# Performance work log

Hardware: AMD Instinct MI355X
Metric: run time of the kernel (lower is better)

The kernel has to match this reference:

```python
import jax, jax.numpy as jnp
import numpy as np

B, T, D, H, C = 256, 512, 300, 128, 6

def setup_inputs() -> dict:
    key = jax.random.key(0)
    ks = jax.random.split(key, 8)
    s = 1.0 / np.sqrt(H)  # PyTorch LSTM/Linear uniform init scale
    x = jax.random.normal(ks[0], (B, T, D), dtype=jnp.float32)
    lengths = jax.random.randint(ks[1], (B,), 1, T + 1)
    W_ih = jax.random.uniform(ks[2], (4 * H, D), minval=-s, maxval=s, dtype=jnp.float32)
    W_hh = jax.random.uniform(ks[3], (4 * H, H), minval=-s, maxval=s, dtype=jnp.float32)
    b_ih = jax.random.uniform(ks[4], (4 * H,), minval=-s, maxval=s, dtype=jnp.float32)
    b_hh = jax.random.uniform(ks[5], (4 * H,), minval=-s, maxval=s, dtype=jnp.float32)
    fc_w = jax.random.uniform(ks[6], (C, H), minval=-s, maxval=s, dtype=jnp.float32)
    fc_b = jax.random.uniform(ks[7], (C,), minval=-s, maxval=s, dtype=jnp.float32)
    return {"x": x, "W_ih": W_ih, "W_hh": W_hh, "b_ih": b_ih, "b_hh": b_hh,
            "fc_w": fc_w, "fc_b": fc_b, "lengths": lengths}

def _lstm_last_hidden(x, W_ih, W_hh, b_ih, b_hh, lengths):
    # Equivalent to pack_padded_sequence + nn.LSTM: the returned hidden[-1]
    # is the state at t = length-1 for each sequence. We run a masked scan:
    # state updates are frozen once t >= length.
    Bv, Tv, _ = x.shape
    Hv = W_hh.shape[1]
    xs = jnp.swapaxes(x, 0, 1)                              # [T, B, D]
    gx = jnp.einsum('tbd,gd->tbg', xs, W_ih) + b_ih + b_hh  # [T, B, 4H]
    mask = (jnp.arange(Tv)[:, None] < lengths[None, :])     # [T, B]

    def step(carry, inp):
        h, c = carry
        g, m = inp
        gates = g + h @ W_hh.T                              # [B, 4H]
        i, f, gg, o = jnp.split(gates, 4, axis=-1)          # PyTorch gate order i,f,g,o
        i = jax.nn.sigmoid(i)
        f = jax.nn.sigmoid(f)
        gg = jnp.tanh(gg)
        o = jax.nn.sigmoid(o)
        c_new = f * c + i * gg
        h_new = o * jnp.tanh(c_new)
        m = m[:, None]
        h = jnp.where(m, h_new, h)
        c = jnp.where(m, c_new, c)
        return (h, c), None

    h0 = jnp.zeros((Bv, Hv), dtype=x.dtype)
    c0 = jnp.zeros((Bv, Hv), dtype=x.dtype)
    (h, c), _ = jax.lax.scan(step, (h0, c0), (gx, mask))
    return h

def reference(x, W_ih, W_hh, b_ih, b_hh, fc_w, fc_b, lengths):
    h = _lstm_last_hidden(x, W_ih, W_hh, b_ih, b_hh, lengths)  # [B, H]
    return h @ fc_w.T + fc_b                                   # [B, 6]
```

## Files before the change

### kernel.cpp

```cpp
#include <hip/hip_runtime.h>
#include <hip/hip_bf16.h>
#include <stdint.h>
#include <type_traits>

#define NB 256
#define NT 512
#define ND 300
#define NH 128
#define NG 512
#define NC 6

typedef __attribute__((ext_vector_type(8))) short short8;
typedef __attribute__((ext_vector_type(4))) float f32x4;

#if __has_builtin(__builtin_amdgcn_fdot2_f32_bf16)
#define HAS_DOT2 1
typedef __attribute__((ext_vector_type(2))) __bf16 bf16x2_t;
static __device__ __forceinline__ float dot2bf(unsigned int wp, unsigned int hp, float acc) {
  return __builtin_amdgcn_fdot2_f32_bf16(__builtin_bit_cast(bf16x2_t, wp),
                                         __builtin_bit_cast(bf16x2_t, hp), acc, false);
}
#else
static __device__ __forceinline__ float dot2bf(unsigned int wp, unsigned int hp, float acc) {
  float wl = __builtin_bit_cast(float, wp << 16);
  float wh = __builtin_bit_cast(float, wp & 0xffff0000u);
  float hl = __builtin_bit_cast(float, hp << 16);
  float hh = __builtin_bit_cast(float, hp & 0xffff0000u);
  return fmaf(wh, hh, fmaf(wl, hl, acc));
}
#endif

static __device__ __forceinline__ float bf2f(unsigned int u) {
  return __builtin_bit_cast(float, (u & 0xffffu) << 16);
}
static __device__ __forceinline__ unsigned short f2bf(float f) {
  return __builtin_bit_cast(unsigned short, __float2bfloat16(f));
}
static __device__ __forceinline__ unsigned int packbf(float a, float b) {
  return (unsigned int)f2bf(a) | ((unsigned int)f2bf(b) << 16);
}
static __device__ __forceinline__ float ld1(const unsigned short* p) { return bf2f(*p); }
static __device__ __forceinline__ float ld1(const float* p) { return *p; }
static __device__ __forceinline__ void st1(unsigned short* p, float v) { *p = f2bf(v); }
static __device__ __forceinline__ void st1(float* p, float v) { *p = v; }

static __device__ __forceinline__ float tanh_fast(float x) {
  return 1.f - 2.f * __builtin_amdgcn_rcpf(__expf(2.f * x) + 1.f);
}

static __device__ __forceinline__ uint2 load4bf(const unsigned short* row, int k, int lim) {
  uint2 v;
  if (k + 3 < lim) {
    v = *(const uint2*)(row + k);
  } else {
    unsigned int e0 = (k + 0 < lim) ? row[k + 0] : 0;
    unsigned int e1 = (k + 1 < lim) ? row[k + 1] : 0;
    unsigned int e2 = (k + 2 < lim) ? row[k + 2] : 0;
    unsigned int e3 = (k + 3 < lim) ? row[k + 3] : 0;
    v.x = e0 | (e1 << 16);
    v.y = e2 | (e3 << 16);
  }
  return v;
}
static __device__ __forceinline__ uint2 load4bf(const float* row, int k, int lim) {
  float f0 = 0.f, f1 = 0.f, f2 = 0.f, f3 = 0.f;
  if (k + 3 < lim) {
    float4 f = *(const float4*)(row + k);
    f0 = f.x; f1 = f.y; f2 = f.z; f3 = f.w;
  } else {
    if (k + 0 < lim) f0 = row[k + 0];
    if (k + 1 < lim) f1 = row[k + 1];
    if (k + 2 < lim) f2 = row[k + 2];
    if (k + 3 < lim) f3 = row[k + 3];
  }
  uint2 v;
  v.x = packbf(f0, f1);
  v.y = packbf(f2, f3);
  return v;
}

__global__ void detect_dtype(const unsigned short* __restrict__ X, int* __restrict__ flag) {
  __shared__ int cnt;
  if (threadIdx.x == 0) cnt = 0;
  __syncthreads();
  int c = 0;
  for (int i = threadIdx.x; i < 512; i += 64) {
    unsigned int u = X[i];
    unsigned int e = (u >> 7) & 0xffu;
    if (u == 0u || (e >= 97u && e <= 157u)) c++;
  }
  atomicAdd(&cnt, c);
  __syncthreads();
  if (threadIdx.x == 0) *flag = (cnt >= 448) ? 0 : 1;
}

template <typename XT, typename GXT>
__global__ __launch_bounds__(256) void gx_gemm(const int* __restrict__ flag, int want,
                                               const XT* __restrict__ X,
                                               const XT* __restrict__ Wih,
                                               const int* __restrict__ lengths,
                                               GXT* __restrict__ gx,
                                               int b_base, int t_base, int Tc) {
  if (*flag != want) return;
  const int mb = blockIdx.x;
  const int m0 = mb << 7;
  const int bc = m0 / Tc;
  const int trel0 = m0 % Tc;
  const int b = b_base + bc;
  const int t0 = t_base + trel0;
  const int len = lengths[b];
  if (t0 >= len) return;

  __shared__ unsigned short As[128][40];
  __shared__ unsigned short Bs[64][40];

  const int tid = threadIdx.x;
  const int lane = tid & 63;
  const int wave = tid >> 6;
  const int wm = wave & 1;
  const int wn = wave >> 1;
  const int lq = lane >> 4;
  const int lr = lane & 15;

  const int rA = tid >> 1, cA = (tid & 1) * 16;
  const int rB = tid >> 2, cB = (tid & 3) * 8;
  const XT* xrow = X + ((size_t)b * NT + t0 + rA) * ND;

  for (int nt = 0; nt < 8; ++nt) {
    const int n0 = nt << 6;
    const XT* wrow = Wih + (size_t)(n0 + rB) * ND;

    f32x4 acc[4][2];
#pragma unroll
    for (int i = 0; i < 4; ++i)
#pragma unroll
      for (int j = 0; j < 2; ++j) {
        f32x4 z = {0.f, 0.f, 0.f, 0.f};
        acc[i][j] = z;
      }

    for (int kc = 0; kc < 320; kc += 32) {
      __syncthreads();
#pragma unroll
      for (int g4 = 0; g4 < 4; ++g4)
        *(uint2*)&As[rA][cA + g4 * 4] = load4bf(xrow, kc + cA + g4 * 4, ND);
#pragma unroll
      for (int g4 = 0; g4 < 2; ++g4)
        *(uint2*)&Bs[rB][cB + g4 * 4] = load4bf(wrow, kc + cB + g4 * 4, ND);
      __syncthreads();

      short8 af[4], bq[2];
#pragma unroll
      for (int tm = 0; tm < 4; ++tm)
        af[tm] = *(const short8*)&As[wm * 64 + tm * 16 + lr][lq * 8];
#pragma unroll
      for (int tn = 0; tn < 2; ++tn)
        bq[tn] = *(const short8*)&Bs[wn * 32 + tn * 16 + lr][lq * 8];
#pragma unroll
      for (int tm = 0; tm < 4; ++tm)
#pragma unroll
        for (int tn = 0; tn < 2; ++tn)
          acc[tm][tn] =
              __builtin_amdgcn_mfma_f32_16x16x32_bf16(af[tm], bq[tn], acc[tm][tn], 0, 0, 0);
    }

#pragma unroll
    for (int tm = 0; tm < 4; ++tm)
#pragma unroll
      for (int tn = 0; tn < 2; ++tn)
#pragma unroll
        for (int rg = 0; rg < 4; ++rg) {
          const int tileRow = wm * 64 + tm * 16 + lq * 4 + rg;
          if (t0 + tileRow < len) {
            const int col = n0 + wn * 32 + tn * 16 + lr;
            st1(gx + (size_t)(m0 + tileRow) * NG + col, acc[tm][tn][rg]);
          }
        }
  }
}

template <typename XT, typename GXT>
__global__ __launch_bounds__(512, 2) void lstm_rec(const int* __restrict__ flag, int want,
                                                   const GXT* __restrict__ gx,
                                                   const XT* __restrict__ Whh,
                                                   const XT* __restrict__ bih,
                                                   const XT* __restrict__ bhh,
                                                   const XT* __restrict__ fcw,
                                                   const XT* __restrict__ fcb,
                                                   const int* __restrict__ lengths,
                                                   XT* __restrict__ out,
                                                   float* __restrict__ hstate,
                                                   float* __restrict__ cstate,
                                                   int b_base, int t_base, int Tc) {
  if (*flag != want) return;
  const int bc = blockIdx.x;
  const int b = b_base + bc;
  int len = lengths[b];
  if (len > NT) len = NT;
  if (len < 0) len = 0;
  const bool first = (t_base == 0);
  const bool last = (t_base + Tc >= NT);
  const int tend = (len < t_base + Tc) ? len : (t_base + Tc);
  if (!last && tend <= t_base) return;

  const int tid = threadIdx.x;
  const int w8 = tid >> 6;
  const int l = tid & 63;
  const int g = l >> 4;
  const int unit = w8 * 16 + (l & 15);
  const int row = g * NH + unit;

  __shared__ __align__(16) unsigned short hpk[2][NH];
  __shared__ __align__(16) float hf[NH];

  unsigned int w2[64];
  if constexpr (std::is_same_v<XT, unsigned short>) {
    const uint4* wp = (const uint4*)Whh + (size_t)row * 16;
#pragma unroll
    for (int i = 0; i < 16; ++i) {
      uint4 v = wp[i];
      w2[4 * i + 0] = v.x;
      w2[4 * i + 1] = v.y;
      w2[4 * i + 2] = v.z;
      w2[4 * i + 3] = v.w;
    }
  } else {
    const float4* wp = (const float4*)(Whh + (size_t)row * NH);
#pragma unroll
    for (int i = 0; i < 32; ++i) {
      float4 v = wp[i];
      w2[2 * i + 0] = packbf(v.x, v.y);
      w2[2 * i + 1] = packbf(v.z, v.w);
    }
  }

  const float bias = ld1(bih + row) + ld1(bhh + row);
  const bool isg = (g == 2);
  const float Au = isg ? 1.f : 0.f;
  const float Bu = isg ? -2.f : 1.f;
  const float Mu = isg ? 2.f : -1.f;

  float hcur = 0.f, ccur = 0.f;
  if (!first) {
    hcur = hstate[(size_t)bc * NH + unit];
    ccur = cstate[(size_t)bc * NH + unit];
  }
  if (g == 0) hpk[0][unit] = f2bf(hcur);
  __syncthreads();

  const GXT* gxc = gx + (size_t)bc * Tc * NG + row;
  const int nsteps = tend - t_base;
  float g_cur = (0 < nsteps) ? ld1(gxc) : 0.f;
  float g_n1 = (1 < nsteps) ? ld1(gxc + NG) : 0.f;

  for (int s = 0; s < nsteps; ++s) {
    float g_n2 = (s + 2 < nsteps) ? ld1(gxc + (size_t)(s + 2) * NG) : 0.f;

    const uint4* hb = (const uint4*)hpk[s & 1];
    float a0 = 0.f, a1 = 0.f, a2 = 0.f, a3 = 0.f;
#pragma unroll
    for (int i = 0; i < 16; ++i) {
      uint4 hv = hb[i];
      a0 = dot2bf(w2[4 * i + 0], hv.x, a0);
      a1 = dot2bf(w2[4 * i + 1], hv.y, a1);
      a2 = dot2bf(w2[4 * i + 2], hv.z, a2);
      a3 = dot2bf(w2[4 * i + 3], hv.w, a3);
    }
    const float gate = g_cur + bias + ((a0 + a1) + (a2 + a3));
    const float v = fmaf(Bu, __builtin_amdgcn_rcpf(__expf(Mu * gate) + 1.f), Au);

    const float x1 = __shfl_xor(v, 16, 64);
    const float x2 = __shfl_xor(v, 32, 64);
    const float x3 = __shfl_xor(x1, 32, 64);
    ccur = fmaf(x1, ccur, v * x2);
    hcur = x3 * tanh_fast(ccur);
    if (g == 0) hpk[(s + 1) & 1][unit] = f2bf(hcur);
    __syncthreads();

    g_cur = g_n1;
    g_n1 = g_n2;
  }

  if (!last) {
    if (g == 0) {
      hstate[(size_t)bc * NH + unit] = hcur;
      cstate[(size_t)bc * NH + unit] = ccur;
    }
  } else {
    if (g == 0) hf[unit] = hcur;
    __syncthreads();
    if (tid < NC) {
      float acc = ld1(fcb + tid);
      const XT* wv = fcw + (size_t)tid * NH;
#pragma unroll
      for (int k = 0; k < NH; ++k) acc = fmaf(ld1(wv + k), hf[k], acc);
      st1(out + (size_t)b * NC + tid, acc);
    }
  }
}

template <typename XT, typename GXT>
static void run_variant(int want, const int* flag, void* const* d_in, XT* out,
                        GXT* gx, float* hstate, float* cstate, int NBc, int Tc,
                        hipStream_t stream) {
  const XT* X = (const XT*)d_in[0];
  const XT* Wih = (const XT*)d_in[1];
  const XT* Whh = (const XT*)d_in[2];
  const XT* bih = (const XT*)d_in[3];
  const XT* bhh = (const XT*)d_in[4];
  const XT* fcw = (const XT*)d_in[5];
  const XT* fcb = (const XT*)d_in[6];
  const int* lengths = (const int*)d_in[7];
  for (int bb = 0; bb < NB; bb += NBc) {
    for (int tb = 0; tb < NT; tb += Tc) {
      gx_gemm<XT, GXT><<<dim3((NBc * Tc) / 128), dim3(256), 0, stream>>>(
          flag, want, X, Wih, lengths, gx, bb, tb, Tc);
      lstm_rec<XT, GXT><<<dim3(NBc), dim3(512), 0, stream>>>(
          flag, want, gx, Whh, bih, bhh, fcw, fcb, lengths, out, hstate, cstate, bb, tb, Tc);
    }
  }
}

extern "C" void kernel_launch(void* const* d_in, const int* in_sizes, int n_in,
                              void* d_out, int out_size, void* d_ws, size_t ws_size,
                              hipStream_t stream) {
  int* flag = (int*)d_ws;
  detect_dtype<<<dim3(1), dim3(64), 0, stream>>>((const unsigned short*)d_in[0], flag);

  const size_t full_f32 = (size_t)NB * NT * NG * sizeof(float);
  const size_t full_bf16 = (size_t)NB * NT * NG * 2;
  const size_t base = 512;

  int NBc, Tc;
  char* gx_raw;
  float* hstate = (float*)((char*)d_ws + base);
  bool gx_is_f32;

  if (ws_size >= base + full_f32) {
    NBc = NB; Tc = NT; gx_is_f32 = true;
    gx_raw = (char*)d_ws + base;
  } else if (ws_size >= base + full_bf16) {
    NBc = NB; Tc = NT; gx_is_f32 = false;
    gx_raw = (char*)d_ws + base;
  } else {
    Tc = 128; gx_is_f32 = false;
    NBc = 1;
    for (int cand : {64, 16, 4}) {
      size_t need = base + (size_t)cand * NH * 2 * sizeof(float) + (size_t)cand * Tc * NG * 2;
      if (ws_size >= need) { NBc = cand; break; }
    }
    gx_raw = (char*)d_ws + base + (size_t)NBc * NH * 2 * sizeof(float);
  }
  float* cstate = hstate + (size_t)NBc * NH;

  if (gx_is_f32) {
    run_variant<unsigned short, float>(0, flag, d_in, (unsigned short*)d_out,
                                       (float*)gx_raw, hstate, cstate, NBc, Tc, stream);
    run_variant<float, float>(1, flag, d_in, (float*)d_out, (float*)gx_raw, hstate,
                              cstate, NBc, Tc, stream);
  } else {
    run_variant<unsigned short, unsigned short>(0, flag, d_in, (unsigned short*)d_out,
                                                (unsigned short*)gx_raw, hstate, cstate,
                                                NBc, Tc, stream);
    run_variant<float, unsigned short>(1, flag, d_in, (float*)d_out,
                                       (unsigned short*)gx_raw, hstate, cstate, NBc, Tc,
                                       stream);
  }
}
```

Baseline: 668.7 us.

## Use MFMA for recurrent h·W_hh matvec and register-prefetch input GEMM tiles

The recurrent step now computes the h·W_hh product with 16x16x32 bf16 MFMA instructions. The W_hh fragments stay in registers, and the broadcast h is the B operand, so 15 of its 16 columns do redundant work. Each lane now holds all four gates for four hidden units, which removes the cross-lane shuffles; gate inputs are loaded as vectors. The input-projection GEMM also prefetches the next K-chunk into registers before the MFMA work, overlapping global loads with compute. This trades dot2 ALU work for wasted MFMA columns and more activation math per lane.

```diff
diff --git a/kernel.cpp b/kernel.cpp
--- a/kernel.cpp
+++ b/kernel.cpp
@@ -13,23 +13,6 @@
 typedef __attribute__((ext_vector_type(8))) short short8;
 typedef __attribute__((ext_vector_type(4))) float f32x4;
 
-#if __has_builtin(__builtin_amdgcn_fdot2_f32_bf16)
-#define HAS_DOT2 1
-typedef __attribute__((ext_vector_type(2))) __bf16 bf16x2_t;
-static __device__ __forceinline__ float dot2bf(unsigned int wp, unsigned int hp, float acc) {
-  return __builtin_amdgcn_fdot2_f32_bf16(__builtin_bit_cast(bf16x2_t, wp),
-                                         __builtin_bit_cast(bf16x2_t, hp), acc, false);
-}
-#else
-static __device__ __forceinline__ float dot2bf(unsigned int wp, unsigned int hp, float acc) {
-  float wl = __builtin_bit_cast(float, wp << 16);
-  float wh = __builtin_bit_cast(float, wp & 0xffff0000u);
-  float hl = __builtin_bit_cast(float, hp << 16);
-  float hh = __builtin_bit_cast(float, hp & 0xffff0000u);
-  return fmaf(wh, hh, fmaf(wl, hl, acc));
-}
-#endif
-
 static __device__ __forceinline__ float bf2f(unsigned int u) {
   return __builtin_bit_cast(float, (u & 0xffffu) << 16);
 }
@@ -44,39 +27,57 @@
 static __device__ __forceinline__ void st1(unsigned short* p, float v) { *p = f2bf(v); }
 static __device__ __forceinline__ void st1(float* p, float v) { *p = v; }
 
+static __device__ __forceinline__ float sigmoid_fast(float x) {
+  return __builtin_amdgcn_rcpf(1.f + __expf(-x));
+}
 static __device__ __forceinline__ float tanh_fast(float x) {
   return 1.f - 2.f * __builtin_amdgcn_rcpf(__expf(2.f * x) + 1.f);
 }
 
+static __device__ __forceinline__ uint2 load4bf_fast(const unsigned short* row, int k) {
+  return *(const uint2*)(row + k);
+}
+static __device__ __forceinline__ uint2 load4bf_fast(const float* row, int k) {
+  float4 f = *(const float4*)(row + k);
+  uint2 v;
+  v.x = packbf(f.x, f.y);
+  v.y = packbf(f.z, f.w);
+  return v;
+}
 static __device__ __forceinline__ uint2 load4bf(const unsigned short* row, int k, int lim) {
+  if (k + 3 < lim) return load4bf_fast(row, k);
+  unsigned int e0 = (k + 0 < lim) ? row[k + 0] : 0;
+  unsigned int e1 = (k + 1 < lim) ? row[k + 1] : 0;
+  unsigned int e2 = (k + 2 < lim) ? row[k + 2] : 0;
+  unsigned int e3 = (k + 3 < lim) ? row[k + 3] : 0;
   uint2 v;
-  if (k + 3 < lim) {
-    v = *(const uint2*)(row + k);
-  } else {
-    unsigned int e0 = (k + 0 < lim) ? row[k + 0] : 0;
-    unsigned int e1 = (k + 1 < lim) ? row[k + 1] : 0;
-    unsigned int e2 = (k + 2 < lim) ? row[k + 2] : 0;
-    unsigned int e3 = (k + 3 < lim) ? row[k + 3] : 0;
-    v.x = e0 | (e1 << 16);
-    v.y = e2 | (e3 << 16);
-  }
+  v.x = e0 | (e1 << 16);
+  v.y = e2 | (e3 << 16);
   return v;
 }
 static __device__ __forceinline__ uint2 load4bf(const float* row, int k, int lim) {
-  float f0 = 0.f, f1 = 0.f, f2 = 0.f, f3 = 0.f;
-  if (k + 3 < lim) {
-    float4 f = *(const float4*)(row + k);
-    f0 = f.x; f1 = f.y; f2 = f.z; f3 = f.w;
-  } else {
-    if (k + 0 < lim) f0 = row[k + 0];
-    if (k + 1 < lim) f1 = row[k + 1];
-    if (k + 2 < lim) f2 = row[k + 2];
-    if (k + 3 < lim) f3 = row[k + 3];
-  }
+  if (k + 3 < lim) return load4bf_fast(row, k);
+  float f0 = (k + 0 < lim) ? row[k + 0] : 0.f;
+  float f1 = (k + 1 < lim) ? row[k + 1] : 0.f;
+  float f2 = (k + 2 < lim) ? row[k + 2] : 0.f;
+  float f3 = (k + 3 < lim) ? row[k + 3] : 0.f;
   uint2 v;
   v.x = packbf(f0, f1);
   v.y = packbf(f2, f3);
   return v;
+}
+
+static __device__ __forceinline__ f32x4 ldgx4(const unsigned short* p) {
+  uint2 v = *(const uint2*)p;
+  f32x4 r;
+  r[0] = bf2f(v.x);
+  r[1] = bf2f(v.x >> 16);
+  r[2] = bf2f(v.y);
+  r[3] = bf2f(v.y >> 16);
+  return r;
+}
+static __device__ __forceinline__ f32x4 ldgx4(const float* p) {
+  return *(const f32x4*)p;
 }
 
 __global__ void detect_dtype(const unsigned short* __restrict__ X, int* __restrict__ flag) {
@@ -139,15 +140,35 @@
         acc[i][j] = z;
       }
 
-    for (int kc = 0; kc < 320; kc += 32) {
+    uint2 av[4], bv[2];
+#pragma unroll
+    for (int g4 = 0; g4 < 4; ++g4) av[g4] = load4bf_fast(xrow, cA + g4 * 4);
+#pragma unroll
+    for (int g4 = 0; g4 < 2; ++g4) bv[g4] = load4bf_fast(wrow, cB + g4 * 4);
+
+#pragma unroll
+    for (int kc9 = 0; kc9 < 10; ++kc9) {
       __syncthreads();
 #pragma unroll
-      for (int g4 = 0; g4 < 4; ++g4)
-        *(uint2*)&As[rA][cA + g4 * 4] = load4bf(xrow, kc + cA + g4 * 4, ND);
-#pragma unroll
-      for (int g4 = 0; g4 < 2; ++g4)
-        *(uint2*)&Bs[rB][cB + g4 * 4] = load4bf(wrow, kc + cB + g4 * 4, ND);
+      for (int g4 = 0; g4 < 4; ++g4) *(uint2*)&As[rA][cA + g4 * 4] = av[g4];
+#pragma unroll
+      for (int g4 = 0; g4 < 2; ++g4) *(uint2*)&Bs[rB][cB + g4 * 4] = bv[g4];
       __syncthreads();
+
+      if (kc9 < 9) {
+        const int kn = (kc9 + 1) * 32;
+        if (kc9 < 8) {
+#pragma unroll
+          for (int g4 = 0; g4 < 4; ++g4) av[g4] = load4bf_fast(xrow, kn + cA + g4 * 4);
+#pragma unroll
+          for (int g4 = 0; g4 < 2; ++g4) bv[g4] = load4bf_fast(wrow, kn + cB + g4 * 4);
+        } else {
+#pragma unroll
+          for (int g4 = 0; g4 < 4; ++g4) av[g4] = load4bf(xrow, kn + cA + g4 * 4, ND);
+#pragma unroll
+          for (int g4 = 0; g4 < 2; ++g4) bv[g4] = load4bf(wrow, kn + cB + g4 * 4, ND);
+        }
+      }
 
       short8 af[4], bq[2];
 #pragma unroll
@@ -202,92 +223,137 @@
   const bool last = (t_base + Tc >= NT);
   const int tend = (len < t_base + Tc) ? len : (t_base + Tc);
   if (!last && tend <= t_base) return;
+  int nsteps = tend - t_base;
+  if (nsteps < 0) nsteps = 0;
 
   const int tid = threadIdx.x;
   const int w8 = tid >> 6;
   const int l = tid & 63;
-  const int g = l >> 4;
-  const int unit = w8 * 16 + (l & 15);
-  const int row = g * NH + unit;
+  const int q = l >> 4;
+  const int m = l & 15;
+  const int u0 = w8 * 16 + q * 4;
 
   __shared__ __align__(16) unsigned short hpk[2][NH];
   __shared__ __align__(16) float hf[NH];
 
-  unsigned int w2[64];
-  if constexpr (std::is_same_v<XT, unsigned short>) {
-    const uint4* wp = (const uint4*)Whh + (size_t)row * 16;
-#pragma unroll
-    for (int i = 0; i < 16; ++i) {
-      uint4 v = wp[i];
-      w2[4 * i + 0] = v.x;
-      w2[4 * i + 1] = v.y;
-      w2[4 * i + 2] = v.z;
-      w2[4 * i + 3] = v.w;
-    }
+  short8 afr[4][4];
+#pragma unroll
+  for (int g = 0; g < 4; ++g) {
+    const int row = g * NH + w8 * 16 + m;
+    if constexpr (std::is_same_v<XT, unsigned short>) {
+#pragma unroll
+      for (int c = 0; c < 4; ++c)
+        afr[g][c] = *(const short8*)(Whh + (size_t)row * NH + c * 32 + q * 8);
+    } else {
+#pragma unroll
+      for (int c = 0; c < 4; ++c) {
+        const float* p = Whh + (size_t)row * NH + c * 32 + q * 8;
+        float4 f0 = *(const float4*)p;
+        float4 f1 = *(const float4*)(p + 4);
+        union { unsigned int u[4]; short8 s; } cv;
+        cv.u[0] = packbf(f0.x, f0.y);
+        cv.u[1] = packbf(f0.z, f0.w);
+        cv.u[2] = packbf(f1.x, f1.y);
+        cv.u[3] = packbf(f1.z, f1.w);
+        afr[g][c] = cv.s;
+      }
+    }
+  }
+
+  f32x4 biasv[4];
+#pragma unroll
+  for (int g = 0; g < 4; ++g)
+#pragma unroll
+    for (int r = 0; r < 4; ++r)
+      biasv[g][r] = ld1(bih + g * NH + u0 + r) + ld1(bhh + g * NH + u0 + r);
+
+  f32x4 cv, hv;
+  if (!first) {
+    hv = *(const f32x4*)&hstate[(size_t)bc * NH + u0];
+    cv = *(const f32x4*)&cstate[(size_t)bc * NH + u0];
   } else {
-    const float4* wp = (const float4*)(Whh + (size_t)row * NH);
-#pragma unroll
-    for (int i = 0; i < 32; ++i) {
-      float4 v = wp[i];
-      w2[2 * i + 0] = packbf(v.x, v.y);
-      w2[2 * i + 1] = packbf(v.z, v.w);
-    }
-  }
-
-  const float bias = ld1(bih + row) + ld1(bhh + row);
-  const bool isg = (g == 2);
-  const float Au = isg ? 1.f : 0.f;
-  const float Bu = isg ? -2.f : 1.f;
-  const float Mu = isg ? 2.f : -1.f;
-
-  float hcur = 0.f, ccur = 0.f;
-  if (!first) {
-    hcur = hstate[(size_t)bc * NH + unit];
-    ccur = cstate[(size_t)bc * NH + unit];
-  }
-  if (g == 0) hpk[0][unit] = f2bf(hcur);
+    f32x4 z = {0.f, 0.f, 0.f, 0.f};
+    hv = z;
+    cv = z;
+  }
+  if (m == 0) {
+    uint2 hp;
+    hp.x = packbf(hv[0], hv[1]);
+    hp.y = packbf(hv[2], hv[3]);
+    *(uint2*)&hpk[0][u0] = hp;
+  }
   __syncthreads();
 
-  const GXT* gxc = gx + (size_t)bc * Tc * NG + row;
-  const int nsteps = tend - t_base;
-  float g_cur = (0 < nsteps) ? ld1(gxc) : 0.f;
-  float g_n1 = (1 < nsteps) ? ld1(gxc + NG) : 0.f;
+  const GXT* gxc = gx + (size_t)bc * Tc * NG;
+  f32x4 gc[4], gn[4];
+  {
+    f32x4 z = {0.f, 0.f, 0.f, 0.f};
+#pragma unroll
+    for (int g = 0; g < 4; ++g) {
+      gc[g] = (0 < nsteps) ? ldgx4(gxc + g * NH + u0) : z;
+      gn[g] = (1 < nsteps) ? ldgx4(gxc + NG + g * NH + u0) : z;
+    }
+  }
 
   for (int s = 0; s < nsteps; ++s) {
-    float g_n2 = (s + 2 < nsteps) ? ld1(gxc + (size_t)(s + 2) * NG) : 0.f;
-
-    const uint4* hb = (const uint4*)hpk[s & 1];
-    float a0 = 0.f, a1 = 0.f, a2 = 0.f, a3 = 0.f;
-#pragma unroll
-    for (int i = 0; i < 16; ++i) {
-      uint4 hv = hb[i];
-      a0 = dot2bf(w2[4 * i + 0], hv.x, a0);
-      a1 = dot2bf(w2[4 * i + 1], hv.y, a1);
-      a2 = dot2bf(w2[4 * i + 2], hv.z, a2);
-      a3 = dot2bf(w2[4 * i + 3], hv.w, a3);
-    }
-    const float gate = g_cur + bias + ((a0 + a1) + (a2 + a3));
-    const float v = fmaf(Bu, __builtin_amdgcn_rcpf(__expf(Mu * gate) + 1.f), Au);
-
-    const float x1 = __shfl_xor(v, 16, 64);
-    const float x2 = __shfl_xor(v, 32, 64);
-    const float x3 = __shfl_xor(x1, 32, 64);
-    ccur = fmaf(x1, ccur, v * x2);
-    hcur = x3 * tanh_fast(ccur);
-    if (g == 0) hpk[(s + 1) & 1][unit] = f2bf(hcur);
+    f32x4 gf[4];
+    {
+      f32x4 z = {0.f, 0.f, 0.f, 0.f};
+#pragma unroll
+      for (int g = 0; g < 4; ++g)
+        gf[g] = (s + 2 < nsteps) ? ldgx4(gxc + (size_t)(s + 2) * NG + g * NH + u0) : z;
+    }
+
+    short8 bfr[4];
+    const unsigned short* hrow = hpk[s & 1];
+#pragma unroll
+    for (int c = 0; c < 4; ++c) bfr[c] = *(const short8*)&hrow[c * 32 + q * 8];
+
+    f32x4 acc[4];
+#pragma unroll
+    for (int g = 0; g < 4; ++g) {
+      f32x4 z = {0.f, 0.f, 0.f, 0.f};
+      acc[g] = z;
+#pragma unroll
+      for (int c = 0; c < 4; ++c)
+        acc[g] = __builtin_amdgcn_mfma_f32_16x16x32_bf16(afr[g][c], bfr[c], acc[g], 0, 0, 0);
+    }
+
+#pragma unroll
+    for (int r = 0; r < 4; ++r) {
+      const float pi = acc[0][r] + biasv[0][r] + gc[0][r];
+      const float pf = acc[1][r] + biasv[1][r] + gc[1][r];
+      const float pg = acc[2][r] + biasv[2][r] + gc[2][r];
+      const float po = acc[3][r] + biasv[3][r] + gc[3][r];
+      const float ig = sigmoid_fast(pi);
+      const float fg = sigmoid_fast(pf);
+      const float gg = tanh_fast(pg);
+      const float og = sigmoid_fast(po);
+      cv[r] = fmaf(fg, cv[r], ig * gg);
+      hv[r] = og * tanh_fast(cv[r]);
+    }
+    if (m == 0) {
+      uint2 hp;
+      hp.x = packbf(hv[0], hv[1]);
+      hp.y = packbf(hv[2], hv[3]);
+      *(uint2*)&hpk[(s + 1) & 1][u0] = hp;
+    }
     __syncthreads();
 
-    g_cur = g_n1;
-    g_n1 = g_n2;
+#pragma unroll
+    for (int g = 0; g < 4; ++g) {
+      gc[g] = gn[g];
+      gn[g] = gf[g];
+    }
   }
 
   if (!last) {
-    if (g == 0) {
-      hstate[(size_t)bc * NH + unit] = hcur;
-      cstate[(size_t)bc * NH + unit] = ccur;
+    if (m == 0) {
+      *(f32x4*)&hstate[(size_t)bc * NH + u0] = hv;
+      *(f32x4*)&cstate[(size_t)bc * NH + u0] = cv;
     }
   } else {
-    if (g == 0) hf[unit] = hcur;
+    if (m == 0) *(f32x4*)&hf[u0] = hv;
     __syncthreads();
     if (tid < NC) {
       float acc = ld1(fcb + tid);
```

New measurement: 938.1 us. 40.3% more time.
